# Kernel optimization log

Measured on AMD Instinct MI355X. Metric: run time of the kernel, lower is better.

The kernel has to match this reference:

```python
import jax, jax.numpy as jnp
import numpy as np

BOND_D = 4    # disentangler bond dim (hard-coded 4 in torch init)
BOND_I = 16   # isometry bond dim (bond_dim kwarg)
F = 2         # feature_dim = 2*nCh, nCh=1 -> [x, 1-x] embedding
LEVELS = [128, 64, 32, 16, 8, 4]
NUM_CLASSES = 10
BATCH = 16


def setup_inputs() -> dict:
    key = jax.random.key(0)
    ks = iter(jax.random.split(key, 128))
    inp = {}
    inp["x"] = jax.random.uniform(next(ks), (BATCH, 1, 128, 128), dtype=jnp.float32)

    def mps_params(P, D, O):
        A = 0.2 * jax.random.normal(next(ks), (P, 4, F, D, D), dtype=jnp.float32)
        v = 0.2 * jax.random.normal(next(ks), (P, D), dtype=jnp.float32)
        w = 0.2 * jax.random.normal(next(ks), (P, D, O), dtype=jnp.float32)
        return A, v, w

    for l, H in enumerate(LEVELS, start=1):
        Pd = ((H - 2) // 2) ** 2   # number of disentangler patches
        Pi = (H // 2) ** 2         # number of isometry patches
        inp[f"d{l}A"], inp[f"d{l}v"], inp[f"d{l}w"] = mps_params(Pd, BOND_D, 4)
        inp[f"i{l}A"], inp[f"i{l}v"], inp[f"i{l}w"] = mps_params(Pi, BOND_I, 1)
    inp["fA"], inp["fv"], inp["fw"] = mps_params(1, BOND_I, NUM_CLASSES)
    return inp


def _patches(x):
    # x: [b, H, W] (H, W even) -> [b, (H/2)*(W/2), 4], same site order as
    # torch unfold(2,2,2).unfold(3,2,2).reshape(..., 4)
    b, H, W = x.shape
    return x.reshape(b, H // 2, 2, W // 2, 2).transpose(0, 1, 3, 2, 4).reshape(b, -1, 4)


def _unpatch(y, nh, nw):
    # y: [b, nh*nw, 4] -> [b, 2*nh, 2*nw], inverse spatial placement of 2x2 blocks
    b = y.shape[0]
    return y.reshape(b, nh, nw, 2, 2).transpose(0, 1, 3, 2, 4).reshape(b, 2 * nh, 2 * nw)


def _mps(patches, A, v, w):
    # Batched per-patch ReLU-MPS over 4 sites.
    # patches [b,P,4], A [P,4,F,D,D], v [P,D], w [P,D,O] -> [b,P,O]
    phi = jnp.stack([patches, 1.0 - patches], axis=-1)          # [b,P,4,F]
    M = jnp.einsum('bpsf,psfij->bpsij', phi, A)                 # [b,P,4,D,D]
    vec = jnp.einsum('pi,bpij->bpj', v, M[:, :, 0])             # [b,P,D]
    for s in range(1, 4):
        vec = jnp.einsum('bpi,bpij->bpj', vec, M[:, :, s])
    return jax.nn.relu(jnp.einsum('bpi,pio->bpo', vec, w))


def _level(x, dA, dv, dw, iA, iv, iw):
    # One MERA layer: disentangle shifted interior patches, write back, then
    # isometry-pool the full grid 2x2 -> 1.
    b, H, W = x.shape
    nh = (H - 2) // 2
    y = _mps(_patches(x[:, 1:-1, 1:-1]), dA, dv, dw)            # [b, nh*nh, 4]
    x = x.at[:, 1:-1, 1:-1].set(_unpatch(y, nh, nh))
    y2 = _mps(_patches(x), iA, iv, iw)                          # [b, (H/2)^2, 1]
    return y2.reshape(b, H // 2, W // 2)


def reference(x, d1A, d1v, d1w, i1A, i1v, i1w,
              d2A, d2v, d2w, i2A, i2v, i2w,
              d3A, d3v, d3w, i3A, i3v, i3w,
              d4A, d4v, d4w, i4A, i4v, i4w,
              d5A, d5v, d5w, i5A, i5v, i5w,
              d6A, d6v, d6w, i6A, i6v, i6w,
              fA, fv, fw):
    h = x[:, 0]  # nCh = 1
    levels = [(d1A, d1v, d1w, i1A, i1v, i1w), (d2A, d2v, d2w, i2A, i2v, i2w),
              (d3A, d3v, d3w, i3A, i3v, i3w), (d4A, d4v, d4w, i4A, i4v, i4w),
              (d5A, d5v, d5w, i5A, i5v, i5w), (d6A, d6v, d6w, i6A, i6v, i6w)]
    for p in levels:
        h = _level(h, *p)
    flat = h.reshape(h.shape[0], 1, 4)         # final 2x2 grid -> 4 sites
    return _mps(flat, fA, fv, fw)[:, 0]        # [b, NUM_CLASSES]
```

## Files before the change

kernel.cpp:

```cpp
#include <hip/hip_runtime.h>

#define BATCH 16

template <int H>
__device__ __forceinline__ float fused_di_unit(
    const float* __restrict__ xb,
    int p, int j,
    const float* __restrict__ dA, const float* __restrict__ dv,
    const float* __restrict__ dw,
    const float* __restrict__ iA, const float* __restrict__ iv,
    const float* __restrict__ iw) {
  constexpr int NH = (H - 2) / 2;
  constexpr int W2 = H / 2;
  int pi = p / W2, pj = p % W2;
  int sg = j >> 2, j4 = j & 3;
  int r = 2 * pi + (sg >> 1), c = 2 * pj + (sg & 1);
  float tcell;
  bool border = (r == 0) | (r == H - 1) | (c == 0) | (c == H - 1);
  if (border) {
    tcell = xb[r * H + c];
  } else {
    int dpi = (r - 1) >> 1, dpj = (c - 1) >> 1;
    int sd = ((r - 1) & 1) * 2 + ((c - 1) & 1);
    int dp = dpi * NH + dpj;
    int R0 = 1 + 2 * dpi, C0 = 1 + 2 * dpj;
    float tin = xb[(R0 + (j4 >> 1)) * H + (C0 + (j4 & 1))];
    const float* Ap = dA + dp * 128;
    float vec = dv[dp * 4 + j4];
#pragma unroll
    for (int s = 0; s < 4; s++) {
      float ts = __shfl(tin, s, 4);
      const float* A0 = Ap + s * 32;
      float q0 = 0.f, q1 = 0.f;
#pragma unroll
      for (int i = 0; i < 4; i++) {
        float sv = __shfl(vec, i, 4);
        q0 = fmaf(sv, A0[i * 4 + j4], q0);
        q1 = fmaf(sv, A0[16 + i * 4 + j4], q1);
      }
      vec = ts * q0 + (1.0f - ts) * q1;
    }
    float y = 0.f;
#pragma unroll
    for (int i = 0; i < 4; i++)
      y = fmaf(__shfl(vec, i, 4), dw[dp * 16 + i * 4 + j4], y);
    y = fmaxf(y, 0.0f);
    tcell = __shfl(y, sd, 4);
  }
  float t[4];
  t[0] = __shfl(tcell, 0, 16);
  t[1] = __shfl(tcell, 4, 16);
  t[2] = __shfl(tcell, 8, 16);
  t[3] = __shfl(tcell, 12, 16);
  const float* Ap = iA + p * 2048;
  float vec = iv[p * 16 + j];
#pragma unroll
  for (int s = 0; s < 4; s++) {
    const float* A0 = Ap + s * 512;
    float q0 = 0.f, q1 = 0.f;
#pragma unroll
    for (int i = 0; i < 16; i++) {
      float sv = __shfl(vec, i, 16);
      q0 = fmaf(sv, A0[i * 16 + j], q0);
      q1 = fmaf(sv, A0[256 + i * 16 + j], q1);
    }
    vec = t[s] * q0 + (1.0f - t[s]) * q1;
  }
  float partial = vec * iw[p * 16 + j];
#pragma unroll
  for (int off = 8; off >= 1; off >>= 1)
    partial += __shfl_xor(partial, off, 16);
  return fmaxf(partial, 0.0f);
}

template <int H>
__global__ __launch_bounds__(256) void level_kernel(
    const float* __restrict__ xin, float* __restrict__ hn,
    const float* __restrict__ dA, const float* __restrict__ dv,
    const float* __restrict__ dw, const float* __restrict__ iA,
    const float* __restrict__ iv, const float* __restrict__ iw) {
  constexpr int W2 = H / 2;
  int g = blockIdx.x * 256 + threadIdx.x;
  int j = g & 15;
  int b = (g >> 4) & 15;
  int p = g >> 8;
  const float* xb = xin + b * H * H;
  float o = fused_di_unit<H>(xb, p, j, dA, dv, dw, iA, iv, iw);
  if (j == 0) hn[b * W2 * W2 + p] = o;
}

struct TailArgs {
  const float* h3;
  const float* in[21];
  float* out;
};

__global__ __launch_bounds__(1024) void tail_kernel(TailArgs a) {
  __shared__ float x4[256];
  __shared__ float h4[64];
  __shared__ float h5[16];
  __shared__ float h6[4];
  int b = blockIdx.x;
  int tid = threadIdx.x;
  if (tid < 256) x4[tid] = a.h3[b * 256 + tid];
  __syncthreads();
  {
    int j = tid & 15, p = tid >> 4;
    float o = fused_di_unit<16>(x4, p, j, a.in[0], a.in[1], a.in[2],
                                a.in[3], a.in[4], a.in[5]);
    if (j == 0) h4[p] = o;
  }
  __syncthreads();
  if (tid < 256) {
    int j = tid & 15, p = tid >> 4;
    float o = fused_di_unit<8>(h4, p, j, a.in[6], a.in[7], a.in[8],
                               a.in[9], a.in[10], a.in[11]);
    if (j == 0) h5[p] = o;
  }
  __syncthreads();
  if (tid < 64) {
    int j = tid & 15, p = tid >> 4;
    float o = fused_di_unit<4>(h5, p, j, a.in[12], a.in[13], a.in[14],
                               a.in[15], a.in[16], a.in[17]);
    if (j == 0) h6[p] = o;
  }
  __syncthreads();
  if (tid < 16) {
    int j = tid;
    const float* fA = a.in[18];
    const float* fv = a.in[19];
    const float* fw = a.in[20];
    float t[4] = {h6[0], h6[1], h6[2], h6[3]};
    float vec = fv[j];
#pragma unroll
    for (int s = 0; s < 4; s++) {
      const float* A0 = fA + s * 512;
      float q0 = 0.f, q1 = 0.f;
#pragma unroll
      for (int i = 0; i < 16; i++) {
        float sv = __shfl(vec, i, 16);
        q0 = fmaf(sv, A0[i * 16 + j], q0);
        q1 = fmaf(sv, A0[256 + i * 16 + j], q1);
      }
      vec = t[s] * q0 + (1.0f - t[s]) * q1;
    }
    float acc = 0.0f;
#pragma unroll
    for (int i = 0; i < 16; i++) {
      float sv = __shfl(vec, i, 16);
      float wv = (j < 10) ? fw[i * 10 + j] : 0.0f;
      acc = fmaf(sv, wv, acc);
    }
    if (j < 10) a.out[b * 10 + j] = fmaxf(acc, 0.0f);
  }
}

extern "C" void kernel_launch(void* const* d_in, const int* in_sizes, int n_in,
                              void* d_out, int out_size, void* d_ws, size_t ws_size,
                              hipStream_t stream) {
  const float* x = (const float*)d_in[0];
  float* ws = (float*)d_ws;
  float* h1 = ws;
  float* h2 = h1 + 65536;
  float* h3 = h2 + 16384;

  level_kernel<128><<<64 * 64, 256, 0, stream>>>(
      x, h1, (const float*)d_in[1], (const float*)d_in[2],
      (const float*)d_in[3], (const float*)d_in[4], (const float*)d_in[5],
      (const float*)d_in[6]);
  level_kernel<64><<<32 * 32, 256, 0, stream>>>(
      h1, h2, (const float*)d_in[7], (const float*)d_in[8],
      (const float*)d_in[9], (const float*)d_in[10], (const float*)d_in[11],
      (const float*)d_in[12]);
  level_kernel<32><<<16 * 16, 256, 0, stream>>>(
      h2, h3, (const float*)d_in[13], (const float*)d_in[14],
      (const float*)d_in[15], (const float*)d_in[16], (const float*)d_in[17],
      (const float*)d_in[18]);

  TailArgs ta;
  ta.h3 = h3;
  for (int i = 0; i < 21; i++) ta.in[i] = (const float*)d_in[19 + i];
  ta.out = (float*)d_out;
  tail_kernel<<<BATCH, 1024, 0, stream>>>(ta);
}
```

Baseline: 216.8 us.

## Use 4 threads per MPS unit with float4 vectorized weight loads

Replaces the 16-lanes-per-(patch,batch) mapping in the first three levels with 4 lanes per unit. Each lane now computes one full disentangler MPS serially and four output components of the isometry chain, loading weights as float4. This cuts shuffle traffic and the thread count by four, and widens memory accesses. The cost is more registers and serial work per thread, plus fewer blocks on the smaller levels, which can reduce occupancy.

```diff
diff --git a/kernel.cpp b/kernel.cpp
--- a/kernel.cpp
+++ b/kernel.cpp
@@ -1,11 +1,120 @@
 #include <hip/hip_runtime.h>
 
 #define BATCH 16
+
+template <int H>
+__device__ __forceinline__ float fused_di_unit4(
+    const float* __restrict__ xb, int p, int q,
+    const float* __restrict__ dA, const float* __restrict__ dv,
+    const float* __restrict__ dw,
+    const float* __restrict__ iA, const float* __restrict__ iv,
+    const float* __restrict__ iw) {
+  constexpr int NH = (H - 2) / 2;
+  constexpr int W2 = H / 2;
+  int pi = p / W2, pj = p % W2;
+  int r = 2 * pi + (q >> 1), c = 2 * pj + (q & 1);
+  float tcell;
+  bool border = (r == 0) | (r == H - 1) | (c == 0) | (c == H - 1);
+  if (border) {
+    tcell = xb[r * H + c];
+  } else {
+    int dpi = (r - 1) >> 1, dpj = (c - 1) >> 1;
+    int sd = ((r - 1) & 1) * 2 + ((c - 1) & 1);
+    int dp = dpi * NH + dpj;
+    int R0 = 1 + 2 * dpi, C0 = 1 + 2 * dpj;
+    float tt[4];
+    tt[0] = xb[R0 * H + C0];
+    tt[1] = xb[R0 * H + C0 + 1];
+    tt[2] = xb[(R0 + 1) * H + C0];
+    tt[3] = xb[(R0 + 1) * H + C0 + 1];
+    const float4* Ad = (const float4*)(dA + dp * 128);
+    float ve[4];
+#pragma unroll
+    for (int i = 0; i < 4; i++) ve[i] = dv[dp * 4 + i];
+#pragma unroll
+    for (int s = 0; s < 4; s++) {
+      float ts = tt[s], us = 1.0f - ts;
+      float vn[4] = {0.f, 0.f, 0.f, 0.f};
+#pragma unroll
+      for (int i = 0; i < 4; i++) {
+        float4 a0 = Ad[s * 8 + i];
+        float4 a1 = Ad[s * 8 + 4 + i];
+        vn[0] = fmaf(ve[i], ts * a0.x + us * a1.x, vn[0]);
+        vn[1] = fmaf(ve[i], ts * a0.y + us * a1.y, vn[1]);
+        vn[2] = fmaf(ve[i], ts * a0.z + us * a1.z, vn[2]);
+        vn[3] = fmaf(ve[i], ts * a0.w + us * a1.w, vn[3]);
+      }
+#pragma unroll
+      for (int i = 0; i < 4; i++) ve[i] = vn[i];
+    }
+    float y = 0.f;
+#pragma unroll
+    for (int i = 0; i < 4; i++) y = fmaf(ve[i], dw[dp * 16 + i * 4 + sd], y);
+    tcell = fmaxf(y, 0.0f);
+  }
+  float t[4];
+  t[0] = __shfl(tcell, 0, 4);
+  t[1] = __shfl(tcell, 1, 4);
+  t[2] = __shfl(tcell, 2, 4);
+  t[3] = __shfl(tcell, 3, 4);
+  const float* Ai = iA + p * 2048;
+  float4 vec = ((const float4*)(iv + p * 16))[q];
+#pragma unroll
+  for (int s = 0; s < 4; s++) {
+    const float4* A0 = (const float4*)(Ai + s * 512);
+    const float4* A1 = (const float4*)(Ai + s * 512 + 256);
+    float ts = t[s], us = 1.0f - ts;
+    float4 q0 = {0.f, 0.f, 0.f, 0.f};
+    float4 q1 = {0.f, 0.f, 0.f, 0.f};
+#pragma unroll
+    for (int i = 0; i < 16; i++) {
+      float comp = ((i & 3) == 0) ? vec.x
+                 : ((i & 3) == 1) ? vec.y
+                 : ((i & 3) == 2) ? vec.z : vec.w;
+      float sv = __shfl(comp, i >> 2, 4);
+      float4 a0 = A0[i * 4 + q];
+      float4 a1 = A1[i * 4 + q];
+      q0.x = fmaf(sv, a0.x, q0.x);
+      q0.y = fmaf(sv, a0.y, q0.y);
+      q0.z = fmaf(sv, a0.z, q0.z);
+      q0.w = fmaf(sv, a0.w, q0.w);
+      q1.x = fmaf(sv, a1.x, q1.x);
+      q1.y = fmaf(sv, a1.y, q1.y);
+      q1.z = fmaf(sv, a1.z, q1.z);
+      q1.w = fmaf(sv, a1.w, q1.w);
+    }
+    vec.x = ts * q0.x + us * q1.x;
+    vec.y = ts * q0.y + us * q1.y;
+    vec.z = ts * q0.z + us * q1.z;
+    vec.w = ts * q0.w + us * q1.w;
+  }
+  float4 w4 = ((const float4*)(iw + p * 16))[q];
+  float partial = vec.x * w4.x + vec.y * w4.y + vec.z * w4.z + vec.w * w4.w;
+  partial += __shfl_xor(partial, 1, 4);
+  partial += __shfl_xor(partial, 2, 4);
+  return fmaxf(partial, 0.0f);
+}
+
+template <int H>
+__global__ __launch_bounds__(256) void level_kernel4(
+    const float* __restrict__ xin, float* __restrict__ hn,
+    const float* __restrict__ dA, const float* __restrict__ dv,
+    const float* __restrict__ dw, const float* __restrict__ iA,
+    const float* __restrict__ iv, const float* __restrict__ iw) {
+  constexpr int W2 = H / 2;
+  int g = blockIdx.x * 256 + threadIdx.x;
+  int q = g & 3;
+  int unit = g >> 2;
+  int b = unit & 15;
+  int p = unit >> 4;
+  const float* xb = xin + b * H * H;
+  float o = fused_di_unit4<H>(xb, p, q, dA, dv, dw, iA, iv, iw);
+  if (q == 0) hn[b * W2 * W2 + p] = o;
+}
 
 template <int H>
 __device__ __forceinline__ float fused_di_unit(
-    const float* __restrict__ xb,
-    int p, int j,
+    const float* __restrict__ xb, int p, int j,
     const float* __restrict__ dA, const float* __restrict__ dv,
     const float* __restrict__ dw,
     const float* __restrict__ iA, const float* __restrict__ iv,
@@ -73,22 +182,6 @@
   return fmaxf(partial, 0.0f);
 }
 
-template <int H>
-__global__ __launch_bounds__(256) void level_kernel(
-    const float* __restrict__ xin, float* __restrict__ hn,
-    const float* __restrict__ dA, const float* __restrict__ dv,
-    const float* __restrict__ dw, const float* __restrict__ iA,
-    const float* __restrict__ iv, const float* __restrict__ iw) {
-  constexpr int W2 = H / 2;
-  int g = blockIdx.x * 256 + threadIdx.x;
-  int j = g & 15;
-  int b = (g >> 4) & 15;
-  int p = g >> 8;
-  const float* xb = xin + b * H * H;
-  float o = fused_di_unit<H>(xb, p, j, dA, dv, dw, iA, iv, iw);
-  if (j == 0) hn[b * W2 * W2 + p] = o;
-}
-
 struct TailArgs {
   const float* h3;
   const float* in[21];
@@ -164,15 +257,15 @@
   float* h2 = h1 + 65536;
   float* h3 = h2 + 16384;
 
-  level_kernel<128><<<64 * 64, 256, 0, stream>>>(
+  level_kernel4<128><<<1024, 256, 0, stream>>>(
       x, h1, (const float*)d_in[1], (const float*)d_in[2],
       (const float*)d_in[3], (const float*)d_in[4], (const float*)d_in[5],
       (const float*)d_in[6]);
-  level_kernel<64><<<32 * 32, 256, 0, stream>>>(
+  level_kernel4<64><<<256, 256, 0, stream>>>(
       h1, h2, (const float*)d_in[7], (const float*)d_in[8],
       (const float*)d_in[9], (const float*)d_in[10], (const float*)d_in[11],
       (const float*)d_in[12]);
-  level_kernel<32><<<16 * 16, 256, 0, stream>>>(
+  level_kernel4<32><<<64, 256, 0, stream>>>(
       h2, h3, (const float*)d_in[13], (const float*)d_in[14],
       (const float*)d_in[15], (const float*)d_in[16], (const float*)d_in[17],
       (const float*)d_in[18]);
```

Measured after the change: 227.6 us. 1.05x slower.
